# Kernel optimization log

Hardware: AMD Instinct MI355X
Metric: run time of the kernel (lower is better)

## Reference

```python
import jax, jax.numpy as jnp
import numpy as np

N = 100000          # nodes
E = 3200000         # edges
C_IN = 64
HIDDEN = 64
NUM_CLASSES = 10
NUM_GRAPHS = 256
EPS = 1e-5


def _graph_conv(x, src, dst, w_rel, w_root, b):
    # PyG GraphConv(aggr='mean'): out_i = W_rel * mean_{j->i} x_j + W_root * x_i + b
    msg_sum = jax.ops.segment_sum(x[src], dst, num_segments=N)            # [N, C]
    cnt = jax.ops.segment_sum(jnp.ones((src.shape[0], 1), x.dtype), dst,
                              num_segments=N)                             # [N, 1]
    agg = msg_sum / jnp.maximum(cnt, 1.0)
    return agg @ w_rel + x @ w_root + b


def _batch_norm(x, gamma, beta):
    # PyG BatchNorm in training mode: batch stats over the node dimension
    mean = jnp.mean(x, axis=0)
    var = jnp.var(x, axis=0)
    return (x - mean) * jax.lax.rsqrt(var + EPS) * gamma + beta


def setup_inputs() -> dict:
    key = jax.random.key(0)
    ks = jax.random.split(key, 20)
    x = jax.random.normal(ks[0], (N, C_IN), dtype=jnp.float32)
    edge_index = jax.random.randint(ks[1], (2, E), 0, N, dtype=jnp.int32)
    batch = jnp.sort(jax.random.randint(ks[2], (N,), 0, NUM_GRAPHS, dtype=jnp.int32))

    def lin(k, fan_in, fan_out):
        s = 1.0 / np.sqrt(fan_in)
        return jax.random.uniform(k, (fan_in, fan_out), jnp.float32, -s, s)

    dims = [(C_IN, 16), (16, 32), (32, 32), (32, HIDDEN)]
    params = {}
    ki = 3
    for i, (ci, co) in enumerate(dims, start=1):
        params[f"w_rel{i}"] = lin(ks[ki], ci, co); ki += 1
        params[f"w_root{i}"] = lin(ks[ki], ci, co); ki += 1
        params[f"b{i}"] = jnp.zeros((co,), jnp.float32)
        params[f"g{i}"] = jnp.ones((co,), jnp.float32)
        params[f"be{i}"] = jnp.zeros((co,), jnp.float32)
    params["w_lin1"] = lin(ks[ki], HIDDEN, HIDDEN); ki += 1
    params["b_lin1"] = jnp.zeros((HIDDEN,), jnp.float32)
    params["w_lin2"] = lin(ks[ki], HIDDEN, NUM_CLASSES); ki += 1
    params["b_lin2"] = jnp.zeros((NUM_CLASSES,), jnp.float32)

    return {"x": x, "edge_index": edge_index, "batch": batch, **params}


def reference(x, edge_index, batch,
              w_rel1, w_root1, b1, g1, be1,
              w_rel2, w_root2, b2, g2, be2,
              w_rel3, w_root3, b3, g3, be3,
              w_rel4, w_root4, b4, g4, be4,
              w_lin1, b_lin1, w_lin2, b_lin2):
    src, dst = edge_index[0], edge_index[1]
    h = jax.nn.elu(_batch_norm(_graph_conv(x, src, dst, w_rel1, w_root1, b1), g1, be1))
    h = jax.nn.elu(_batch_norm(_graph_conv(h, src, dst, w_rel2, w_root2, b2), g2, be2))
    h = jax.nn.elu(_batch_norm(_graph_conv(h, src, dst, w_rel3, w_root3, b3), g3, be3))
    h = jax.nn.elu(_batch_norm(_graph_conv(h, src, dst, w_rel4, w_root4, b4), g4, be4))
    # global mean pool over graphs
    pooled = jax.ops.segment_sum(h, batch, num_segments=NUM_GRAPHS)
    cnt = jax.ops.segment_sum(jnp.ones((N, 1), h.dtype), batch, num_segments=NUM_GRAPHS)
    pooled = pooled / jnp.maximum(cnt, 1.0)
    z = jax.nn.relu(pooled @ w_lin1 + b_lin1)
    # dropout omitted (deterministic / eval mode)
    logits = z @ w_lin2 + b_lin2
    return jax.nn.log_softmax(logits, axis=-1)
```

## Files before the change

kernel.cpp:

```cpp
#include <hip/hip_runtime.h>
#include <hip/hip_bf16.h>
#include <math.h>

#define NGRAPHS 256
#define BSHIFT 8
#define NBUCK 512
#define NSORT 256
#define SBLK 256
#define SMASK 0x00FFFFFFu

__device__ __forceinline__ float bf2f(unsigned short u) {
    return __uint_as_float((unsigned)u << 16);
}
__device__ __forceinline__ unsigned short f2bf(float f) {
    unsigned u = __float_as_uint(f);
    unsigned r = (u + 0x7FFFu + ((u >> 16) & 1u)) >> 16;
    return (unsigned short)r;
}

__global__ __launch_bounds__(256) void k_bhist(const int* __restrict__ dst, int* __restrict__ hmat, int E) {
    __shared__ int hist[NBUCK];
    for (int i = threadIdx.x; i < NBUCK; i += 256) hist[i] = 0;
    __syncthreads();
    int chunk = (E + NSORT - 1) / NSORT;
    int lo = blockIdx.x * chunk;
    int hi = lo + chunk; if (hi > E) hi = E;
    for (int i = lo + threadIdx.x; i < hi; i += 256) {
        int d = __builtin_nontemporal_load(dst + i);
        atomicAdd(&hist[d >> BSHIFT], 1);
    }
    __syncthreads();
    for (int i = threadIdx.x; i < NBUCK; i += 256)
        hmat[(size_t)blockIdx.x * NBUCK + i] = hist[i];
}

__global__ __launch_bounds__(256) void k_cscan(int* __restrict__ hmat, int* __restrict__ btot) {
    int col = blockIdx.x * 256 + threadIdx.x;
    int run = 0;
#pragma unroll 4
    for (int r = 0; r < NSORT; r++) {
        int v = hmat[(size_t)r * NBUCK + col];
        hmat[(size_t)r * NBUCK + col] = run;
        run += v;
    }
    btot[col] = run;
}

__global__ __launch_bounds__(512) void k_bscan(const int* __restrict__ btot, int* __restrict__ bstart) {
    __shared__ int s[512];
    int tid = threadIdx.x;
    int v = btot[tid];
    s[tid] = v;
    __syncthreads();
    for (int off = 1; off < 512; off <<= 1) {
        int t = (tid >= off) ? s[tid - off] : 0;
        __syncthreads();
        s[tid] += t;
        __syncthreads();
    }
    bstart[tid] = s[tid] - v;
    if (tid == 511) bstart[NBUCK] = s[511];
}

__global__ __launch_bounds__(256) void k_bscatter(const int* __restrict__ src, const int* __restrict__ dst,
                                                  const int* __restrict__ hmat, const int* __restrict__ bstart,
                                                  unsigned* __restrict__ ebuf, int E) {
    __shared__ int cur[NBUCK];
    for (int i = threadIdx.x; i < NBUCK; i += 256)
        cur[i] = bstart[i] + hmat[(size_t)blockIdx.x * NBUCK + i];
    __syncthreads();
    int chunk = (E + NSORT - 1) / NSORT;
    int lo = blockIdx.x * chunk;
    int hi = lo + chunk; if (hi > E) hi = E;
    for (int i = lo + threadIdx.x; i < hi; i += 256) {
        int d = __builtin_nontemporal_load(dst + i);
        int s = __builtin_nontemporal_load(src + i);
        int p = atomicAdd(&cur[d >> BSHIFT], 1);
        ebuf[p] = (unsigned)s | ((unsigned)(d & 255) << 24);
    }
}

__global__ __launch_bounds__(256) void k_sort2(const unsigned* __restrict__ ebuf, const int* __restrict__ bstart,
                                               int* __restrict__ csr, int* __restrict__ row_start, int N) {
    __shared__ int hist[256];
    __shared__ int sc[256];
    __shared__ int scur[256];
    int b = blockIdx.x;
    int e0 = bstart[b], e1 = bstart[b + 1];
    hist[threadIdx.x] = 0;
    __syncthreads();
    for (int i = e0 + threadIdx.x; i < e1; i += 256)
        atomicAdd(&hist[__builtin_nontemporal_load(ebuf + i) >> 24], 1);
    __syncthreads();
    sc[threadIdx.x] = hist[threadIdx.x];
    __syncthreads();
    for (int off = 1; off < 256; off <<= 1) {
        int t = (threadIdx.x >= off) ? sc[threadIdx.x - off] : 0;
        __syncthreads();
        sc[threadIdx.x] += t;
        __syncthreads();
    }
    {
        int inc = sc[threadIdx.x];
        int ex = inc - hist[threadIdx.x];
        scur[threadIdx.x] = e0 + ex;
        int node = (b << BSHIFT) + threadIdx.x;
        if (node < N) row_start[node] = e0 + ex;
        if (node == N - 1) row_start[N] = e0 + inc;
    }
    __syncthreads();
    for (int i = e0 + threadIdx.x; i < e1; i += 256) {
        unsigned w = __builtin_nontemporal_load(ebuf + i);
        int p = atomicAdd(&scur[w >> 24], 1);
        csr[p] = (int)(w & SMASK);
    }
}

template <int CI, int CO, bool HAS_REL, bool HAS_ROOT, bool ADD_AGG, bool HAS_BIAS, bool IN_BF16, bool OUT_BF16>
__global__ __launch_bounds__(256) void k_lin(const void* __restrict__ hroot_v, const float* __restrict__ hrel,
                                             const float* __restrict__ w_rel, const float* __restrict__ w_root,
                                             const float* __restrict__ bias, const float* __restrict__ aggadd,
                                             float* __restrict__ out, unsigned short* __restrict__ outb, int N) {
    constexpr int QPR = CO / 4;
    __shared__ float s_rel[HAS_REL ? CI * CO : 1];
    __shared__ float s_root[HAS_ROOT ? CI * CO : 1];
    __shared__ float s_b[HAS_BIAS ? CO : 4];
    if (HAS_REL)
        for (int i = threadIdx.x; i < CI * CO; i += 256) s_rel[i] = w_rel[i];
    if (HAS_ROOT)
        for (int i = threadIdx.x; i < CI * CO; i += 256) s_root[i] = w_root[i];
    if (HAS_BIAS && threadIdx.x < CO) s_b[threadIdx.x] = bias[threadIdx.x];
    __syncthreads();

    int t = blockIdx.x * 256 + threadIdx.x;
    int n = t / QPR;
    int c0 = (t % QPR) * 4;
    if (n >= N) return;

    float rr[HAS_ROOT ? CI : 1];
    if (HAS_ROOT) {
        if (IN_BF16) {
            const ushort4* hp = (const ushort4*)((const unsigned short*)hroot_v + (size_t)n * CI);
#pragma unroll
            for (int i = 0; i < CI / 4; i++) {
                ushort4 v = hp[i];
                rr[4 * i + 0] = bf2f(v.x); rr[4 * i + 1] = bf2f(v.y);
                rr[4 * i + 2] = bf2f(v.z); rr[4 * i + 3] = bf2f(v.w);
            }
        } else {
            const float4* hp = (const float4*)((const float*)hroot_v + (size_t)n * CI);
#pragma unroll
            for (int i = 0; i < CI / 4; i++) {
                float4 v = hp[i];
                rr[4 * i + 0] = v.x; rr[4 * i + 1] = v.y; rr[4 * i + 2] = v.z; rr[4 * i + 3] = v.w;
            }
        }
    }
    float ar[HAS_REL ? CI : 1];
    if (HAS_REL) {
        const float4* mp = (const float4*)(hrel + (size_t)n * CI);
#pragma unroll
        for (int i = 0; i < CI / 4; i++) {
            float4 v = mp[i];
            ar[4 * i + 0] = v.x; ar[4 * i + 1] = v.y; ar[4 * i + 2] = v.z; ar[4 * i + 3] = v.w;
        }
    }

    float4 acc;
    if (HAS_BIAS) acc = *(const float4*)&s_b[c0];
    else { acc.x = 0.f; acc.y = 0.f; acc.z = 0.f; acc.w = 0.f; }
    if (ADD_AGG) {
        float4 v = *(const float4*)(aggadd + (size_t)n * CO + c0);
        acc.x += v.x; acc.y += v.y; acc.z += v.z; acc.w += v.w;
    }

#pragma unroll
    for (int ci = 0; ci < CI; ci++) {
        if (HAS_REL) {
            float a = ar[ci];
            float4 w = *(const float4*)&s_rel[ci * CO + c0];
            acc.x += a * w.x; acc.y += a * w.y; acc.z += a * w.z; acc.w += a * w.w;
        }
        if (HAS_ROOT) {
            float hv = rr[ci];
            float4 w = *(const float4*)&s_root[ci * CO + c0];
            acc.x += hv * w.x; acc.y += hv * w.y; acc.z += hv * w.z; acc.w += hv * w.w;
        }
    }
    if (OUT_BF16) {
        ushort4 o;
        o.x = f2bf(acc.x); o.y = f2bf(acc.y); o.z = f2bf(acc.z); o.w = f2bf(acc.w);
        *(ushort4*)(outb + (size_t)n * CO + c0) = o;
    } else {
        *(float4*)(out + (size_t)n * CO + c0) = acc;
    }
}

#define GCHUNK 1024
template <int C>
__global__ __launch_bounds__(256) void k_gather(const unsigned short* __restrict__ h,
                                                const int* __restrict__ row_start,
                                                const int* __restrict__ csr, float* __restrict__ agg, int N) {
    constexpr int LPR = C / 4;
    constexpr int EPP = 64 / LPR;
    constexpr int DEPTH = 32 / EPP;
    __shared__ int sbuf[GCHUNK];
    int lane = threadIdx.x & 63;
    int w = threadIdx.x >> 6;
    int nb = blockIdx.x * 4;
    int wid = nb + w;
    bool act = wid < N;
    int nb_end = nb + 4; if (nb_end > N) nb_end = N;
    int eb0 = row_start[nb];
    int eb1 = row_start[nb_end];
    int r0 = act ? row_start[wid] : 0;
    int r1 = act ? row_start[wid + 1] : 0;
    int es = lane / LPR;
    int cq = (lane % LPR) * 4;

    float a0 = 0.f, a1 = 0.f, a2 = 0.f, a3 = 0.f;
    for (int base = eb0; base < eb1; base += GCHUNK) {
        int len = eb1 - base; if (len > GCHUNK) len = GCHUNK;
        __syncthreads();
        for (int i = threadIdx.x; i < len; i += 256)
            sbuf[i] = __builtin_nontemporal_load(csr + base + i);
        __syncthreads();
        if (act) {
            int lo = (r0 > base ? r0 : base) - base;
            int hiv = r1 < base + len ? r1 : base + len;
            int hi = hiv - base;
            if (hi > lo) {
                int nfull = (hi - lo) >> 5;
                int j0 = lo;
                for (int b = 0; b < nfull; b++, j0 += 32) {
                    int s[DEPTH];
#pragma unroll
                    for (int u = 0; u < DEPTH; u++) s[u] = sbuf[j0 + u * EPP + es];
                    ushort4 v[DEPTH];
#pragma unroll
                    for (int u = 0; u < DEPTH; u++)
                        v[u] = *(const ushort4*)(h + (size_t)s[u] * C + cq);
#pragma unroll
                    for (int u = 0; u < DEPTH; u++) {
                        a0 += bf2f(v[u].x); a1 += bf2f(v[u].y);
                        a2 += bf2f(v[u].z); a3 += bf2f(v[u].w);
                    }
                }
                for (int j = j0 + es; j < hi; j += EPP) {
                    int s = sbuf[j];
                    ushort4 v = *(const ushort4*)(h + (size_t)s * C + cq);
                    a0 += bf2f(v.x); a1 += bf2f(v.y); a2 += bf2f(v.z); a3 += bf2f(v.w);
                }
            }
        }
    }
#pragma unroll
    for (int off = LPR; off < 64; off <<= 1) {
        a0 += __shfl_xor(a0, off, 64);
        a1 += __shfl_xor(a1, off, 64);
        a2 += __shfl_xor(a2, off, 64);
        a3 += __shfl_xor(a3, off, 64);
    }
    if (act && lane < LPR) {
        int deg = r1 - r0;
        float rec = 1.0f / (float)(deg > 0 ? deg : 1);
        float4 o; o.x = a0 * rec; o.y = a1 * rec; o.z = a2 * rec; o.w = a3 * rec;
        *(float4*)(agg + (size_t)wid * C + cq) = o;
    }
}

template <int CO>
__global__ __launch_bounds__(256) void k_stats(const float* __restrict__ h, float* __restrict__ partials,
                                               const float* __restrict__ g, const float* __restrict__ be,
                                               float* __restrict__ stats, int* __restrict__ cnt,
                                               float invN, int N) {
    constexpr int QPR = CO / 4;
    __shared__ float part[4][2 * CO];
    __shared__ float red[128];
    __shared__ int is_last;
    int total = N * QPR;
    float s0 = 0, s1 = 0, s2 = 0, s3 = 0, q0 = 0, q1 = 0, q2 = 0, q3 = 0;
    int idx = blockIdx.x * 256 + threadIdx.x;
    for (int i = idx; i < total; i += SBLK * 256) {
        float4 v = ((const float4*)h)[i];
        s0 += v.x; q0 += v.x * v.x;
        s1 += v.y; q1 += v.y * v.y;
        s2 += v.z; q2 += v.z * v.z;
        s3 += v.w; q3 += v.w * v.w;
    }
#pragma unroll
    for (int off = QPR; off < 64; off <<= 1) {
        s0 += __shfl_xor(s0, off, 64); q0 += __shfl_xor(q0, off, 64);
        s1 += __shfl_xor(s1, off, 64); q1 += __shfl_xor(q1, off, 64);
        s2 += __shfl_xor(s2, off, 64); q2 += __shfl_xor(q2, off, 64);
        s3 += __shfl_xor(s3, off, 64); q3 += __shfl_xor(q3, off, 64);
    }
    int lane = threadIdx.x & 63;
    int w = threadIdx.x >> 6;
    if (lane < QPR) {
        int cq = lane * 4;
        part[w][cq + 0] = s0; part[w][CO + cq + 0] = q0;
        part[w][cq + 1] = s1; part[w][CO + cq + 1] = q1;
        part[w][cq + 2] = s2; part[w][CO + cq + 2] = q2;
        part[w][cq + 3] = s3; part[w][CO + cq + 3] = q3;
    }
    __syncthreads();
    if (threadIdx.x < 2 * CO) {
        float v = part[0][threadIdx.x] + part[1][threadIdx.x] + part[2][threadIdx.x] + part[3][threadIdx.x];
        partials[blockIdx.x * (2 * CO) + threadIdx.x] = v;
    }
    __threadfence();
    if (threadIdx.x == 0) is_last = (atomicAdd(cnt, 1) == SBLK - 1);
    __syncthreads();
    if (!is_last) return;
    __threadfence();
    int c = threadIdx.x;
    if (c < 2 * CO) {
        float s = 0.f;
        for (int b = 0; b < SBLK; b++) s += partials[b * 2 * CO + c];
        red[c] = s;
    }
    __syncthreads();
    if (c < CO) {
        float mean = red[c] * invN;
        float var = red[CO + c] * invN - mean * mean;
        float sc = g[c] * rsqrtf(var + 1e-5f);
        stats[128 + c] = sc;
        stats[192 + c] = be[c] - mean * sc;
    }
}

template <int CO>
__global__ __launch_bounds__(256) void k_bn_elu(const float* __restrict__ h, const float* __restrict__ stats,
                                                unsigned short* __restrict__ hb, int N) {
    __shared__ float sc[CO], sh[CO];
    if (threadIdx.x < CO) {
        sc[threadIdx.x] = stats[128 + threadIdx.x];
        sh[threadIdx.x] = stats[192 + threadIdx.x];
    }
    __syncthreads();
    int total = N * (CO / 4);
    int i = blockIdx.x * 256 + threadIdx.x;
    if (i >= total) return;
    float4 v = ((const float4*)h)[i];
    int cq = (i % (CO / 4)) * 4;
    v.x = v.x * sc[cq + 0] + sh[cq + 0];
    v.y = v.y * sc[cq + 1] + sh[cq + 1];
    v.z = v.z * sc[cq + 2] + sh[cq + 2];
    v.w = v.w * sc[cq + 3] + sh[cq + 3];
    v.x = v.x > 0.f ? v.x : expm1f(v.x);
    v.y = v.y > 0.f ? v.y : expm1f(v.y);
    v.z = v.z > 0.f ? v.z : expm1f(v.z);
    v.w = v.w > 0.f ? v.w : expm1f(v.w);
    ushort4 o;
    o.x = f2bf(v.x); o.y = f2bf(v.y); o.z = f2bf(v.z); o.w = f2bf(v.w);
    ((ushort4*)hb)[i] = o;
}

__global__ __launch_bounds__(256) void k_bn_elu_pool(const float* __restrict__ h, const float* __restrict__ stats,
                                                     const int* __restrict__ batch,
                                                     float* __restrict__ pooled, float* __restrict__ cntg, int N) {
    int lane = threadIdx.x & 63;
    int wid = blockIdx.x * 4 + (threadIdx.x >> 6);
    int n0 = wid * 16;
    if (n0 >= N) return;
    float scl = stats[128 + lane];
    float shl = stats[192 + lane];
    int nmax = N - n0; if (nmax > 16) nmax = 16;
    int cur = batch[n0];
    float acc = 0.f;
    float run = 0.f;
    for (int k = 0; k < nmax; k++) {
        int g = batch[n0 + k];
        if (g != cur) {
            atomicAdd(&pooled[(size_t)cur * 64 + lane], acc);
            if (lane == 0) atomicAdd(&cntg[cur], run);
            cur = g; acc = 0.f; run = 0.f;
        }
        float v = h[(size_t)(n0 + k) * 64 + lane] * scl + shl;
        v = v > 0.f ? v : expm1f(v);
        acc += v;
        run += 1.f;
    }
    atomicAdd(&pooled[(size_t)cur * 64 + lane], acc);
    if (lane == 0) atomicAdd(&cntg[cur], run);
}

__global__ __launch_bounds__(256) void k_head(const float* __restrict__ pooled, const float* __restrict__ cntg,
                                              const float* __restrict__ w1, const float* __restrict__ b1,
                                              const float* __restrict__ w2, const float* __restrict__ b2,
                                              float* __restrict__ out) {
    int g = threadIdx.x;
    float rec = 1.0f / fmaxf(cntg[g], 1.0f);
    float p[64];
    {
        const float4* pp = (const float4*)(pooled + (size_t)g * 64);
#pragma unroll
        for (int i = 0; i < 16; i++) {
            float4 v = pp[i];
            p[4 * i + 0] = v.x * rec; p[4 * i + 1] = v.y * rec;
            p[4 * i + 2] = v.z * rec; p[4 * i + 3] = v.w * rec;
        }
    }
    float lg[10];
#pragma unroll
    for (int t = 0; t < 10; t++) lg[t] = b2[t];
#pragma unroll 1
    for (int j = 0; j < 64; j++) {
        float a = b1[j];
#pragma unroll
        for (int k = 0; k < 64; k++) a += p[k] * w1[k * 64 + j];
        a = fmaxf(a, 0.f);
#pragma unroll
        for (int t = 0; t < 10; t++) lg[t] += a * w2[j * 10 + t];
    }
    float m = -1e30f;
#pragma unroll
    for (int t = 0; t < 10; t++) m = fmaxf(m, lg[t]);
    float s = 0.f;
#pragma unroll
    for (int t = 0; t < 10; t++) s += expf(lg[t] - m);
    float lse = m + logf(s);
#pragma unroll
    for (int t = 0; t < 10; t++) out[(size_t)g * 10 + t] = lg[t] - lse;
}

extern "C" void kernel_launch(void* const* d_in, const int* in_sizes, int n_in,
                              void* d_out, int out_size, void* d_ws, size_t ws_size,
                              hipStream_t stream) {
    const float* x = (const float*)d_in[0];
    const int* ei = (const int*)d_in[1];
    const int* batch = (const int*)d_in[2];
    const int N = in_sizes[0] / 64;
    const int E = in_sizes[1] / 2;
    const int* src = ei;
    const int* dst = ei + E;

    const float* w_rel1 = (const float*)d_in[3];
    const float* w_root1 = (const float*)d_in[4];
    const float* b1 = (const float*)d_in[5];
    const float* g1 = (const float*)d_in[6];
    const float* be1 = (const float*)d_in[7];
    const float* w_rel2 = (const float*)d_in[8];
    const float* w_root2 = (const float*)d_in[9];
    const float* b2 = (const float*)d_in[10];
    const float* g2 = (const float*)d_in[11];
    const float* be2 = (const float*)d_in[12];
    const float* w_rel3 = (const float*)d_in[13];
    const float* w_root3 = (const float*)d_in[14];
    const float* b3 = (const float*)d_in[15];
    const float* g3 = (const float*)d_in[16];
    const float* be3 = (const float*)d_in[17];
    const float* w_rel4 = (const float*)d_in[18];
    const float* w_root4 = (const float*)d_in[19];
    const float* b4 = (const float*)d_in[20];
    const float* g4 = (const float*)d_in[21];
    const float* be4 = (const float*)d_in[22];
    const float* w_lin1 = (const float*)d_in[23];
    const float* b_lin1 = (const float*)d_in[24];
    const float* w_lin2 = (const float*)d_in[25];
    const float* b_lin2 = (const float*)d_in[26];

    char* ws = (char*)d_ws;
    size_t off = 0;
    auto alloc = [&](size_t bytes) { size_t o = off; off += (bytes + 255) & ~(size_t)255; return o; };
    int* hmat = (int*)(ws + alloc((size_t)NSORT * NBUCK * 4));
    int* btot = (int*)(ws + alloc((size_t)NBUCK * 4));
    int* bstart = (int*)(ws + alloc((size_t)(NBUCK + 1) * 4));
    unsigned* ebuf = (unsigned*)(ws + alloc((size_t)E * 4));
    int* csr = (int*)(ws + alloc((size_t)E * 4));
    int* row_start = (int*)(ws + alloc((size_t)(N + 1) * 4));
    float* agg = (float*)(ws + alloc((size_t)N * 32 * 4));
    unsigned short* y1b = (unsigned short*)(ws + alloc((size_t)N * 16 * 2));
    unsigned short* hb = (unsigned short*)(ws + alloc((size_t)N * 64 * 2));
    float* bufA = (float*)(ws + alloc((size_t)N * 64 * 4));
    float* stats = (float*)(ws + alloc(4 * 256 * 4));
    float* partials = (float*)(ws + alloc((size_t)SBLK * 128 * 4));
    float* pooled = (float*)(ws + alloc((size_t)(NGRAPHS * 64 + NGRAPHS + 8) * 4));
    float* cntg = pooled + NGRAPHS * 64;
    int* cnt = (int*)(cntg + NGRAPHS);

    hipMemsetAsync(pooled, 0, (size_t)(NGRAPHS * 64 + NGRAPHS + 8) * 4, stream);

    const float invN = 1.0f / (float)N;
    const int gbl = (N + 3) / 4;
    auto lgrid = [&](int qpr) { return (N * qpr + 255) / 256; };

    k_bhist<<<NSORT, 256, 0, stream>>>(dst, hmat, E);
    k_cscan<<<NBUCK / 256, 256, 0, stream>>>(hmat, btot);
    k_bscan<<<1, 512, 0, stream>>>(btot, bstart);
    k_bscatter<<<NSORT, 256, 0, stream>>>(src, dst, hmat, bstart, ebuf, E);
    k_sort2<<<NBUCK, 256, 0, stream>>>(ebuf, bstart, csr, row_start, N);

    k_lin<64, 16, true, false, false, false, false, true><<<lgrid(4), 256, 0, stream>>>(
        nullptr, x, w_rel1, nullptr, nullptr, nullptr, nullptr, y1b, N);
    k_gather<16><<<gbl, 256, 0, stream>>>(y1b, row_start, csr, agg, N);
    k_lin<64, 16, false, true, true, true, false, false><<<lgrid(4), 256, 0, stream>>>(
        x, nullptr, nullptr, w_root1, b1, agg, bufA, nullptr, N);
    k_stats<16><<<SBLK, 256, 0, stream>>>(bufA, partials, g1, be1, stats + 0, cnt + 0, invN, N);
    k_bn_elu<16><<<(N * 4 + 255) / 256, 256, 0, stream>>>(bufA, stats + 0, hb, N);

    k_gather<16><<<gbl, 256, 0, stream>>>(hb, row_start, csr, agg, N);
    k_lin<16, 32, true, true, false, true, true, false><<<lgrid(8), 256, 0, stream>>>(
        hb, agg, w_rel2, w_root2, b2, nullptr, bufA, nullptr, N);
    k_stats<32><<<SBLK, 256, 0, stream>>>(bufA, partials, g2, be2, stats + 256, cnt + 1, invN, N);
    k_bn_elu<32><<<(N * 8 + 255) / 256, 256, 0, stream>>>(bufA, stats + 256, hb, N);

    k_gather<32><<<gbl, 256, 0, stream>>>(hb, row_start, csr, agg, N);
    k_lin<32, 32, true, true, false, true, true, false><<<lgrid(8), 256, 0, stream>>>(
        hb, agg, w_rel3, w_root3, b3, nullptr, bufA, nullptr, N);
    k_stats<32><<<SBLK, 256, 0, stream>>>(bufA, partials, g3, be3, stats + 512, cnt + 2, invN, N);
    k_bn_elu<32><<<(N * 8 + 255) / 256, 256, 0, stream>>>(bufA, stats + 512, hb, N);

    k_gather<32><<<gbl, 256, 0, stream>>>(hb, row_start, csr, agg, N);
    k_lin<32, 64, true, true, false, true, true, false><<<lgrid(16), 256, 0, stream>>>(
        hb, agg, w_rel4, w_root4, b4, nullptr, bufA, nullptr, N);
    k_stats<64><<<SBLK, 256, 0, stream>>>(bufA, partials, g4, be4, stats + 768, cnt + 3, invN, N);
    int waves16 = (N + 15) / 16;
    k_bn_elu_pool<<<(waves16 + 3) / 4, 256, 0, stream>>>(bufA, stats + 768, batch, pooled, cntg, N);

    k_head<<<1, 256, 0, stream>>>(pooled, cntg, w_lin1, b_lin1, w_lin2, b_lin2, (float*)d_out);
}
```

Baseline: 638.9 us.

## Fuse whole GNN pipeline into one cooperative persistent kernel with grid syncs

Replaces the chain of about twenty separate kernel launches with a single cooperative persistent megakernel. Phases (bucket sort, CSR build, linear layers, gathers, batch-norm stats, pooling, head) are separated by grid-wide syncs, and blocks loop over work with grid stride. The per-call memset is folded into the first phase, and the batch-norm statistics appear to be merged into the linear phases. This removes launch gaps and tail idle time, at the cost of grid-sync overhead and occupancy-limited persistent grids, with a multi-kernel fallback when cooperative launch is unavailable.

```diff
diff --git a/kernel.cpp b/kernel.cpp
--- a/kernel.cpp
+++ b/kernel.cpp
@@ -1,12 +1,15 @@
 #include <hip/hip_runtime.h>
+#include <hip/hip_cooperative_groups.h>
 #include <hip/hip_bf16.h>
 #include <math.h>
+
+namespace cg = cooperative_groups;
 
 #define NGRAPHS 256
 #define BSHIFT 8
 #define NBUCK 512
 #define NSORT 256
-#define SBLK 256
+#define GCHUNK 1024
 #define SMASK 0x00FFFFFFu
 
 __device__ __forceinline__ float bf2f(unsigned short u) {
@@ -18,275 +21,289 @@
     return (unsigned short)r;
 }
 
-__global__ __launch_bounds__(256) void k_bhist(const int* __restrict__ dst, int* __restrict__ hmat, int E) {
-    __shared__ int hist[NBUCK];
-    for (int i = threadIdx.x; i < NBUCK; i += 256) hist[i] = 0;
-    __syncthreads();
-    int chunk = (E + NSORT - 1) / NSORT;
-    int lo = blockIdx.x * chunk;
-    int hi = lo + chunk; if (hi > E) hi = E;
-    for (int i = lo + threadIdx.x; i < hi; i += 256) {
-        int d = __builtin_nontemporal_load(dst + i);
-        atomicAdd(&hist[d >> BSHIFT], 1);
-    }
-    __syncthreads();
-    for (int i = threadIdx.x; i < NBUCK; i += 256)
-        hmat[(size_t)blockIdx.x * NBUCK + i] = hist[i];
-}
-
-__global__ __launch_bounds__(256) void k_cscan(int* __restrict__ hmat, int* __restrict__ btot) {
-    int col = blockIdx.x * 256 + threadIdx.x;
-    int run = 0;
-#pragma unroll 4
+struct SMLin { float rel[2048]; float root[2048]; float b[64]; float part[512]; };
+struct SMSort { int h[256]; int s[256]; int c[256]; };
+struct SMBn { float sc[64]; float sh[64]; };
+union SM {
+    int hist[NBUCK];
+    int sbuf[GCHUNK];
+    int scan[512];
+    SMSort sort;
+    SMLin lin;
+    SMBn bn;
+};
+
+struct MegaP {
+    const float* x; const int* src; const int* dst; const int* batch;
+    int N, E; float invN;
+    const float *w_rel1, *w_root1, *b1, *g1, *be1;
+    const float *w_rel2, *w_root2, *b2, *g2, *be2;
+    const float *w_rel3, *w_root3, *b3, *g3, *be3;
+    const float *w_rel4, *w_root4, *b4, *g4, *be4;
+    const float *w_lin1, *b_lin1, *w_lin2, *b_lin2;
+    int* hmat; int* bstart; unsigned* ebuf; int* csr; int* row_start;
+    float* agg; unsigned short* y1b; unsigned short* hb; float* bufA;
+    float* gs;
+    float* pooled; float* cntg;
+    float* out;
+};
+
+__device__ void phA(const MegaP& p, SM* sm) {
+    int bid = blockIdx.x, tid = threadIdx.x;
+    if (bid < NSORT) {
+        for (int i = tid; i < NBUCK; i += 256) sm->hist[i] = 0;
+        __syncthreads();
+        int chunk = (p.E + NSORT - 1) / NSORT;
+        int lo = bid * chunk;
+        int hi = lo + chunk; if (hi > p.E) hi = p.E;
+        for (int i = lo + tid; i < hi; i += 256)
+            atomicAdd(&sm->hist[__builtin_nontemporal_load(p.dst + i) >> BSHIFT], 1);
+        __syncthreads();
+        for (int i = tid; i < NBUCK; i += 256)
+            p.hmat[(size_t)bid * NBUCK + i] = sm->hist[i];
+    } else {
+        if (bid == NSORT) {
+            for (int i = tid; i < NGRAPHS * 64 + NGRAPHS; i += 256) p.pooled[i] = 0.f;
+            for (int i = tid; i < 512; i += 256) p.gs[i] = 0.f;
+        }
+        float* s_rel = sm->lin.rel;
+        for (int i = tid; i < 64 * 16; i += 256) s_rel[i] = p.w_rel1[i];
+        __syncthreads();
+        int total = p.N * 4;
+        int nb = gridDim.x - NSORT;
+        for (int i = (bid - NSORT) * 256 + tid; i < total; i += nb * 256) {
+            int n = i >> 2, c0 = (i & 3) << 2;
+            const float4* mp = (const float4*)(p.x + (size_t)n * 64);
+            float4 acc; acc.x = 0.f; acc.y = 0.f; acc.z = 0.f; acc.w = 0.f;
+#pragma unroll
+            for (int k2 = 0; k2 < 16; k2++) {
+                float4 v = mp[k2];
+                const float* wr = &s_rel[(k2 * 4) * 16 + c0];
+                float4 w0 = *(const float4*)(wr);
+                float4 w1 = *(const float4*)(wr + 16);
+                float4 w2 = *(const float4*)(wr + 32);
+                float4 w3 = *(const float4*)(wr + 48);
+                acc.x += v.x * w0.x + v.y * w1.x + v.z * w2.x + v.w * w3.x;
+                acc.y += v.x * w0.y + v.y * w1.y + v.z * w2.y + v.w * w3.y;
+                acc.z += v.x * w0.z + v.y * w1.z + v.z * w2.z + v.w * w3.z;
+                acc.w += v.x * w0.w + v.y * w1.w + v.z * w2.w + v.w * w3.w;
+            }
+            ushort4 o; o.x = f2bf(acc.x); o.y = f2bf(acc.y); o.z = f2bf(acc.z); o.w = f2bf(acc.w);
+            *(ushort4*)(p.y1b + (size_t)n * 16 + c0) = o;
+        }
+    }
+}
+
+__device__ void phB(const MegaP& p, SM* sm) {
+    int t = threadIdx.x;
+    int run0 = 0, run1 = 0;
     for (int r = 0; r < NSORT; r++) {
-        int v = hmat[(size_t)r * NBUCK + col];
-        hmat[(size_t)r * NBUCK + col] = run;
-        run += v;
-    }
-    btot[col] = run;
-}
-
-__global__ __launch_bounds__(512) void k_bscan(const int* __restrict__ btot, int* __restrict__ bstart) {
-    __shared__ int s[512];
-    int tid = threadIdx.x;
-    int v = btot[tid];
-    s[tid] = v;
-    __syncthreads();
-    for (int off = 1; off < 512; off <<= 1) {
-        int t = (tid >= off) ? s[tid - off] : 0;
-        __syncthreads();
-        s[tid] += t;
-        __syncthreads();
-    }
-    bstart[tid] = s[tid] - v;
-    if (tid == 511) bstart[NBUCK] = s[511];
-}
-
-__global__ __launch_bounds__(256) void k_bscatter(const int* __restrict__ src, const int* __restrict__ dst,
-                                                  const int* __restrict__ hmat, const int* __restrict__ bstart,
-                                                  unsigned* __restrict__ ebuf, int E) {
-    __shared__ int cur[NBUCK];
-    for (int i = threadIdx.x; i < NBUCK; i += 256)
-        cur[i] = bstart[i] + hmat[(size_t)blockIdx.x * NBUCK + i];
-    __syncthreads();
-    int chunk = (E + NSORT - 1) / NSORT;
-    int lo = blockIdx.x * chunk;
-    int hi = lo + chunk; if (hi > E) hi = E;
-    for (int i = lo + threadIdx.x; i < hi; i += 256) {
-        int d = __builtin_nontemporal_load(dst + i);
-        int s = __builtin_nontemporal_load(src + i);
-        int p = atomicAdd(&cur[d >> BSHIFT], 1);
-        ebuf[p] = (unsigned)s | ((unsigned)(d & 255) << 24);
-    }
-}
-
-__global__ __launch_bounds__(256) void k_sort2(const unsigned* __restrict__ ebuf, const int* __restrict__ bstart,
-                                               int* __restrict__ csr, int* __restrict__ row_start, int N) {
-    __shared__ int hist[256];
-    __shared__ int sc[256];
-    __shared__ int scur[256];
-    int b = blockIdx.x;
-    int e0 = bstart[b], e1 = bstart[b + 1];
-    hist[threadIdx.x] = 0;
-    __syncthreads();
-    for (int i = e0 + threadIdx.x; i < e1; i += 256)
-        atomicAdd(&hist[__builtin_nontemporal_load(ebuf + i) >> 24], 1);
-    __syncthreads();
-    sc[threadIdx.x] = hist[threadIdx.x];
+        size_t base = (size_t)r * NBUCK;
+        int v0 = p.hmat[base + t];
+        int v1 = p.hmat[base + 256 + t];
+        p.hmat[base + t] = run0;
+        p.hmat[base + 256 + t] = run1;
+        run0 += v0; run1 += v1;
+    }
+    sm->scan[t] = run0; sm->scan[256 + t] = run1;
     __syncthreads();
     for (int off = 1; off < 256; off <<= 1) {
-        int t = (threadIdx.x >= off) ? sc[threadIdx.x - off] : 0;
-        __syncthreads();
-        sc[threadIdx.x] += t;
-        __syncthreads();
-    }
-    {
-        int inc = sc[threadIdx.x];
-        int ex = inc - hist[threadIdx.x];
-        scur[threadIdx.x] = e0 + ex;
-        int node = (b << BSHIFT) + threadIdx.x;
-        if (node < N) row_start[node] = e0 + ex;
-        if (node == N - 1) row_start[N] = e0 + inc;
-    }
-    __syncthreads();
-    for (int i = e0 + threadIdx.x; i < e1; i += 256) {
-        unsigned w = __builtin_nontemporal_load(ebuf + i);
-        int p = atomicAdd(&scur[w >> 24], 1);
-        csr[p] = (int)(w & SMASK);
-    }
-}
-
-template <int CI, int CO, bool HAS_REL, bool HAS_ROOT, bool ADD_AGG, bool HAS_BIAS, bool IN_BF16, bool OUT_BF16>
-__global__ __launch_bounds__(256) void k_lin(const void* __restrict__ hroot_v, const float* __restrict__ hrel,
-                                             const float* __restrict__ w_rel, const float* __restrict__ w_root,
-                                             const float* __restrict__ bias, const float* __restrict__ aggadd,
-                                             float* __restrict__ out, unsigned short* __restrict__ outb, int N) {
-    constexpr int QPR = CO / 4;
-    __shared__ float s_rel[HAS_REL ? CI * CO : 1];
-    __shared__ float s_root[HAS_ROOT ? CI * CO : 1];
-    __shared__ float s_b[HAS_BIAS ? CO : 4];
-    if (HAS_REL)
-        for (int i = threadIdx.x; i < CI * CO; i += 256) s_rel[i] = w_rel[i];
-    if (HAS_ROOT)
-        for (int i = threadIdx.x; i < CI * CO; i += 256) s_root[i] = w_root[i];
-    if (HAS_BIAS && threadIdx.x < CO) s_b[threadIdx.x] = bias[threadIdx.x];
-    __syncthreads();
-
-    int t = blockIdx.x * 256 + threadIdx.x;
-    int n = t / QPR;
-    int c0 = (t % QPR) * 4;
-    if (n >= N) return;
-
-    float rr[HAS_ROOT ? CI : 1];
-    if (HAS_ROOT) {
-        if (IN_BF16) {
-            const ushort4* hp = (const ushort4*)((const unsigned short*)hroot_v + (size_t)n * CI);
-#pragma unroll
-            for (int i = 0; i < CI / 4; i++) {
-                ushort4 v = hp[i];
-                rr[4 * i + 0] = bf2f(v.x); rr[4 * i + 1] = bf2f(v.y);
-                rr[4 * i + 2] = bf2f(v.z); rr[4 * i + 3] = bf2f(v.w);
-            }
-        } else {
-            const float4* hp = (const float4*)((const float*)hroot_v + (size_t)n * CI);
-#pragma unroll
-            for (int i = 0; i < CI / 4; i++) {
-                float4 v = hp[i];
-                rr[4 * i + 0] = v.x; rr[4 * i + 1] = v.y; rr[4 * i + 2] = v.z; rr[4 * i + 3] = v.w;
-            }
-        }
-    }
-    float ar[HAS_REL ? CI : 1];
-    if (HAS_REL) {
-        const float4* mp = (const float4*)(hrel + (size_t)n * CI);
-#pragma unroll
-        for (int i = 0; i < CI / 4; i++) {
-            float4 v = mp[i];
-            ar[4 * i + 0] = v.x; ar[4 * i + 1] = v.y; ar[4 * i + 2] = v.z; ar[4 * i + 3] = v.w;
-        }
-    }
-
-    float4 acc;
-    if (HAS_BIAS) acc = *(const float4*)&s_b[c0];
-    else { acc.x = 0.f; acc.y = 0.f; acc.z = 0.f; acc.w = 0.f; }
-    if (ADD_AGG) {
-        float4 v = *(const float4*)(aggadd + (size_t)n * CO + c0);
-        acc.x += v.x; acc.y += v.y; acc.z += v.z; acc.w += v.w;
-    }
-
-#pragma unroll
-    for (int ci = 0; ci < CI; ci++) {
-        if (HAS_REL) {
-            float a = ar[ci];
-            float4 w = *(const float4*)&s_rel[ci * CO + c0];
-            acc.x += a * w.x; acc.y += a * w.y; acc.z += a * w.z; acc.w += a * w.w;
-        }
-        if (HAS_ROOT) {
-            float hv = rr[ci];
-            float4 w = *(const float4*)&s_root[ci * CO + c0];
-            acc.x += hv * w.x; acc.y += hv * w.y; acc.z += hv * w.z; acc.w += hv * w.w;
-        }
-    }
-    if (OUT_BF16) {
-        ushort4 o;
-        o.x = f2bf(acc.x); o.y = f2bf(acc.y); o.z = f2bf(acc.z); o.w = f2bf(acc.w);
-        *(ushort4*)(outb + (size_t)n * CO + c0) = o;
-    } else {
-        *(float4*)(out + (size_t)n * CO + c0) = acc;
-    }
-}
-
-#define GCHUNK 1024
+        int v0 = (t >= off) ? sm->scan[t - off] : 0;
+        int v1 = (t >= off) ? sm->scan[256 + t - off] : 0;
+        __syncthreads();
+        sm->scan[t] += v0; sm->scan[256 + t] += v1;
+        __syncthreads();
+    }
+    int lowtot = sm->scan[255];
+    int incU = sm->scan[256 + t] + lowtot;
+    p.bstart[t] = sm->scan[t] - run0;
+    p.bstart[256 + t] = incU - run1;
+    if (t == 255) p.bstart[NBUCK] = incU;
+}
+
+__device__ void phC(const MegaP& p, SM* sm) {
+    int tid = threadIdx.x;
+    for (int b = blockIdx.x; b < NSORT; b += gridDim.x) {
+        for (int i = tid; i < NBUCK; i += 256)
+            sm->hist[i] = p.bstart[i] + p.hmat[(size_t)b * NBUCK + i];
+        __syncthreads();
+        int chunk = (p.E + NSORT - 1) / NSORT;
+        int lo = b * chunk;
+        int hi = lo + chunk; if (hi > p.E) hi = p.E;
+        for (int i = lo + tid; i < hi; i += 256) {
+            int d = __builtin_nontemporal_load(p.dst + i);
+            int s = __builtin_nontemporal_load(p.src + i);
+            int pos = atomicAdd(&sm->hist[d >> BSHIFT], 1);
+            p.ebuf[pos] = (unsigned)s | ((unsigned)(d & 255) << 24);
+        }
+        __syncthreads();
+    }
+}
+
+__device__ void phD(const MegaP& p, SM* sm) {
+    int tid = threadIdx.x;
+    for (int b = blockIdx.x; b < NBUCK; b += gridDim.x) {
+        int e0 = p.bstart[b], e1 = p.bstart[b + 1];
+        sm->sort.h[tid] = 0;
+        __syncthreads();
+        for (int i = e0 + tid; i < e1; i += 256)
+            atomicAdd(&sm->sort.h[__builtin_nontemporal_load(p.ebuf + i) >> 24], 1);
+        __syncthreads();
+        sm->sort.s[tid] = sm->sort.h[tid];
+        __syncthreads();
+        for (int off = 1; off < 256; off <<= 1) {
+            int v = (tid >= off) ? sm->sort.s[tid - off] : 0;
+            __syncthreads();
+            sm->sort.s[tid] += v;
+            __syncthreads();
+        }
+        {
+            int inc = sm->sort.s[tid];
+            int ex = inc - sm->sort.h[tid];
+            sm->sort.c[tid] = e0 + ex;
+            int node = (b << BSHIFT) + tid;
+            if (node < p.N) p.row_start[node] = e0 + ex;
+            if (node == p.N - 1) p.row_start[p.N] = e0 + inc;
+        }
+        __syncthreads();
+        for (int i = e0 + tid; i < e1; i += 256) {
+            unsigned w = __builtin_nontemporal_load(p.ebuf + i);
+            int pos = atomicAdd(&sm->sort.c[w >> 24], 1);
+            p.csr[pos] = (int)(w & SMASK);
+        }
+        __syncthreads();
+    }
+}
+
 template <int C>
-__global__ __launch_bounds__(256) void k_gather(const unsigned short* __restrict__ h,
-                                                const int* __restrict__ row_start,
-                                                const int* __restrict__ csr, float* __restrict__ agg, int N) {
+__device__ void ph_gather(const MegaP& p, SM* sm, const unsigned short* h) {
     constexpr int LPR = C / 4;
     constexpr int EPP = 64 / LPR;
     constexpr int DEPTH = 32 / EPP;
-    __shared__ int sbuf[GCHUNK];
     int lane = threadIdx.x & 63;
     int w = threadIdx.x >> 6;
-    int nb = blockIdx.x * 4;
-    int wid = nb + w;
-    bool act = wid < N;
-    int nb_end = nb + 4; if (nb_end > N) nb_end = N;
-    int eb0 = row_start[nb];
-    int eb1 = row_start[nb_end];
-    int r0 = act ? row_start[wid] : 0;
-    int r1 = act ? row_start[wid + 1] : 0;
     int es = lane / LPR;
     int cq = (lane % LPR) * 4;
-
-    float a0 = 0.f, a1 = 0.f, a2 = 0.f, a3 = 0.f;
-    for (int base = eb0; base < eb1; base += GCHUNK) {
-        int len = eb1 - base; if (len > GCHUNK) len = GCHUNK;
-        __syncthreads();
-        for (int i = threadIdx.x; i < len; i += 256)
-            sbuf[i] = __builtin_nontemporal_load(csr + base + i);
-        __syncthreads();
-        if (act) {
-            int lo = (r0 > base ? r0 : base) - base;
-            int hiv = r1 < base + len ? r1 : base + len;
-            int hi = hiv - base;
-            if (hi > lo) {
-                int nfull = (hi - lo) >> 5;
-                int j0 = lo;
-                for (int b = 0; b < nfull; b++, j0 += 32) {
-                    int s[DEPTH];
-#pragma unroll
-                    for (int u = 0; u < DEPTH; u++) s[u] = sbuf[j0 + u * EPP + es];
-                    ushort4 v[DEPTH];
-#pragma unroll
-                    for (int u = 0; u < DEPTH; u++)
-                        v[u] = *(const ushort4*)(h + (size_t)s[u] * C + cq);
-#pragma unroll
-                    for (int u = 0; u < DEPTH; u++) {
-                        a0 += bf2f(v[u].x); a1 += bf2f(v[u].y);
-                        a2 += bf2f(v[u].z); a3 += bf2f(v[u].w);
+    int ngrp = (p.N + 3) >> 2;
+    for (int grp = blockIdx.x; grp < ngrp; grp += gridDim.x) {
+        int nb = grp * 4;
+        int wid = nb + w;
+        bool act = wid < p.N;
+        int nb_end = nb + 4; if (nb_end > p.N) nb_end = p.N;
+        int eb0 = p.row_start[nb];
+        int eb1 = p.row_start[nb_end];
+        int r0 = act ? p.row_start[wid] : 0;
+        int r1 = act ? p.row_start[wid + 1] : 0;
+        float a0 = 0.f, a1 = 0.f, a2 = 0.f, a3 = 0.f;
+        for (int base = eb0; base < eb1; base += GCHUNK) {
+            int len = eb1 - base; if (len > GCHUNK) len = GCHUNK;
+            __syncthreads();
+            for (int i = threadIdx.x; i < len; i += 256)
+                sm->sbuf[i] = __builtin_nontemporal_load(p.csr + base + i);
+            __syncthreads();
+            if (act) {
+                int lo = (r0 > base ? r0 : base) - base;
+                int hiv = r1 < base + len ? r1 : base + len;
+                int hi = hiv - base;
+                if (hi > lo) {
+                    int nfull = (hi - lo) >> 5;
+                    int j0 = lo;
+                    for (int bb = 0; bb < nfull; bb++, j0 += 32) {
+                        int s[DEPTH];
+#pragma unroll
+                        for (int u = 0; u < DEPTH; u++) s[u] = sm->sbuf[j0 + u * EPP + es];
+                        ushort4 v[DEPTH];
+#pragma unroll
+                        for (int u = 0; u < DEPTH; u++)
+                            v[u] = *(const ushort4*)(h + (size_t)s[u] * C + cq);
+#pragma unroll
+                        for (int u = 0; u < DEPTH; u++) {
+                            a0 += bf2f(v[u].x); a1 += bf2f(v[u].y);
+                            a2 += bf2f(v[u].z); a3 += bf2f(v[u].w);
+                        }
+                    }
+                    for (int j = j0 + es; j < hi; j += EPP) {
+                        int s = sm->sbuf[j];
+                        ushort4 v = *(const ushort4*)(h + (size_t)s * C + cq);
+                        a0 += bf2f(v.x); a1 += bf2f(v.y); a2 += bf2f(v.z); a3 += bf2f(v.w);
                     }
                 }
-                for (int j = j0 + es; j < hi; j += EPP) {
-                    int s = sbuf[j];
-                    ushort4 v = *(const ushort4*)(h + (size_t)s * C + cq);
-                    a0 += bf2f(v.x); a1 += bf2f(v.y); a2 += bf2f(v.z); a3 += bf2f(v.w);
-                }
             }
         }
-    }
-#pragma unroll
-    for (int off = LPR; off < 64; off <<= 1) {
-        a0 += __shfl_xor(a0, off, 64);
-        a1 += __shfl_xor(a1, off, 64);
-        a2 += __shfl_xor(a2, off, 64);
-        a3 += __shfl_xor(a3, off, 64);
-    }
-    if (act && lane < LPR) {
-        int deg = r1 - r0;
-        float rec = 1.0f / (float)(deg > 0 ? deg : 1);
-        float4 o; o.x = a0 * rec; o.y = a1 * rec; o.z = a2 * rec; o.w = a3 * rec;
-        *(float4*)(agg + (size_t)wid * C + cq) = o;
-    }
-}
-
-template <int CO>
-__global__ __launch_bounds__(256) void k_stats(const float* __restrict__ h, float* __restrict__ partials,
-                                               const float* __restrict__ g, const float* __restrict__ be,
-                                               float* __restrict__ stats, int* __restrict__ cnt,
-                                               float invN, int N) {
+#pragma unroll
+        for (int off = LPR; off < 64; off <<= 1) {
+            a0 += __shfl_xor(a0, off, 64);
+            a1 += __shfl_xor(a1, off, 64);
+            a2 += __shfl_xor(a2, off, 64);
+            a3 += __shfl_xor(a3, off, 64);
+        }
+        if (act && lane < LPR) {
+            int deg = r1 - r0;
+            float rec = 1.0f / (float)(deg > 0 ? deg : 1);
+            float4 o; o.x = a0 * rec; o.y = a1 * rec; o.z = a2 * rec; o.w = a3 * rec;
+            *(float4*)(p.agg + (size_t)wid * C + cq) = o;
+        }
+    }
+}
+
+template <int CI, int CO, bool HAS_REL, bool ADD_AGG, bool IN_BF16>
+__device__ void ph_lin_stats(const MegaP& p, SM* sm, const void* hroot_v, const float* hrel,
+                             const float* w_rel, const float* w_root, const float* bias,
+                             float* out, float* gsl) {
     constexpr int QPR = CO / 4;
-    __shared__ float part[4][2 * CO];
-    __shared__ float red[128];
-    __shared__ int is_last;
-    int total = N * QPR;
+    int tid = threadIdx.x;
+    if (HAS_REL)
+        for (int i = tid; i < CI * CO; i += 256) sm->lin.rel[i] = w_rel[i];
+    for (int i = tid; i < CI * CO; i += 256) sm->lin.root[i] = w_root[i];
+    if (tid < CO) sm->lin.b[tid] = bias[tid];
+    __syncthreads();
+    int total = p.N * QPR;
+    int stride = gridDim.x * 256;
     float s0 = 0, s1 = 0, s2 = 0, s3 = 0, q0 = 0, q1 = 0, q2 = 0, q3 = 0;
-    int idx = blockIdx.x * 256 + threadIdx.x;
-    for (int i = idx; i < total; i += SBLK * 256) {
-        float4 v = ((const float4*)h)[i];
-        s0 += v.x; q0 += v.x * v.x;
-        s1 += v.y; q1 += v.y * v.y;
-        s2 += v.z; q2 += v.z * v.z;
-        s3 += v.w; q3 += v.w * v.w;
+    for (int i = blockIdx.x * 256 + tid; i < total; i += stride) {
+        int n = i / QPR, c0 = (i % QPR) * 4;
+        float4 acc = *(const float4*)&sm->lin.b[c0];
+        if (ADD_AGG) {
+            float4 v = ((const float4*)p.agg)[i];
+            acc.x += v.x; acc.y += v.y; acc.z += v.z; acc.w += v.w;
+        }
+#pragma unroll
+        for (int cb = 0; cb < CI / 4; cb++) {
+            float f0, f1, f2, f3;
+            if (IN_BF16) {
+                ushort4 v = *(const ushort4*)((const unsigned short*)hroot_v + (size_t)n * CI + cb * 4);
+                f0 = bf2f(v.x); f1 = bf2f(v.y); f2 = bf2f(v.z); f3 = bf2f(v.w);
+            } else {
+                float4 v = *(const float4*)((const float*)hroot_v + (size_t)n * CI + cb * 4);
+                f0 = v.x; f1 = v.y; f2 = v.z; f3 = v.w;
+            }
+            const float* wr = &sm->lin.root[(cb * 4) * CO + c0];
+            float4 w0 = *(const float4*)(wr);
+            float4 w1 = *(const float4*)(wr + CO);
+            float4 w2 = *(const float4*)(wr + 2 * CO);
+            float4 w3 = *(const float4*)(wr + 3 * CO);
+            acc.x += f0 * w0.x + f1 * w1.x + f2 * w2.x + f3 * w3.x;
+            acc.y += f0 * w0.y + f1 * w1.y + f2 * w2.y + f3 * w3.y;
+            acc.z += f0 * w0.z + f1 * w1.z + f2 * w2.z + f3 * w3.z;
+            acc.w += f0 * w0.w + f1 * w1.w + f2 * w2.w + f3 * w3.w;
+            if (HAS_REL) {
+                float4 a = *(const float4*)(hrel + (size_t)n * CI + cb * 4);
+                const float* we = &sm->lin.rel[(cb * 4) * CO + c0];
+                float4 e0 = *(const float4*)(we);
+                float4 e1 = *(const float4*)(we + CO);
+                float4 e2 = *(const float4*)(we + 2 * CO);
+                float4 e3 = *(const float4*)(we + 3 * CO);
+                acc.x += a.x * e0.x + a.y * e1.x + a.z * e2.x + a.w * e3.x;
+                acc.y += a.x * e0.y + a.y * e1.y + a.z * e2.y + a.w * e3.y;
+                acc.z += a.x * e0.z + a.y * e1.z + a.z * e2.z + a.w * e3.z;
+                acc.w += a.x * e0.w + a.y * e1.w + a.z * e2.w + a.w * e3.w;
+            }
+        }
+        ((float4*)out)[i] = acc;
+        s0 += acc.x; q0 += acc.x * acc.x;
+        s1 += acc.y; q1 += acc.y * acc.y;
+        s2 += acc.z; q2 += acc.z * acc.z;
+        s3 += acc.w; q3 += acc.w * acc.w;
     }
 #pragma unroll
     for (int off = QPR; off < 64; off <<= 1) {
@@ -295,124 +312,115 @@
         s2 += __shfl_xor(s2, off, 64); q2 += __shfl_xor(q2, off, 64);
         s3 += __shfl_xor(s3, off, 64); q3 += __shfl_xor(q3, off, 64);
     }
-    int lane = threadIdx.x & 63;
-    int w = threadIdx.x >> 6;
+    int lane = tid & 63;
+    int w = tid >> 6;
     if (lane < QPR) {
         int cq = lane * 4;
-        part[w][cq + 0] = s0; part[w][CO + cq + 0] = q0;
-        part[w][cq + 1] = s1; part[w][CO + cq + 1] = q1;
-        part[w][cq + 2] = s2; part[w][CO + cq + 2] = q2;
-        part[w][cq + 3] = s3; part[w][CO + cq + 3] = q3;
+        float* pr = &sm->lin.part[w * 2 * CO];
+        pr[cq + 0] = s0; pr[CO + cq + 0] = q0;
+        pr[cq + 1] = s1; pr[CO + cq + 1] = q1;
+        pr[cq + 2] = s2; pr[CO + cq + 2] = q2;
+        pr[cq + 3] = s3; pr[CO + cq + 3] = q3;
     }
     __syncthreads();
-    if (threadIdx.x < 2 * CO) {
-        float v = part[0][threadIdx.x] + part[1][threadIdx.x] + part[2][threadIdx.x] + part[3][threadIdx.x];
-        partials[blockIdx.x * (2 * CO) + threadIdx.x] = v;
-    }
-    __threadfence();
-    if (threadIdx.x == 0) is_last = (atomicAdd(cnt, 1) == SBLK - 1);
+    if (tid < 2 * CO) {
+        float v = sm->lin.part[tid] + sm->lin.part[2 * CO + tid] +
+                  sm->lin.part[4 * CO + tid] + sm->lin.part[6 * CO + tid];
+        atomicAdd(&gsl[tid], v);
+    }
+}
+
+template <int CO>
+__device__ void ph_bn_elu(const MegaP& p, SM* sm, const float* gsl, const float* g, const float* be) {
+    int tid = threadIdx.x;
+    if (tid < CO) {
+        float mean = gsl[tid] * p.invN;
+        float var = gsl[CO + tid] * p.invN - mean * mean;
+        float sc = g[tid] * rsqrtf(var + 1e-5f);
+        sm->bn.sc[tid] = sc;
+        sm->bn.sh[tid] = be[tid] - mean * sc;
+    }
     __syncthreads();
-    if (!is_last) return;
-    __threadfence();
-    int c = threadIdx.x;
-    if (c < 2 * CO) {
-        float s = 0.f;
-        for (int b = 0; b < SBLK; b++) s += partials[b * 2 * CO + c];
-        red[c] = s;
+    int total = p.N * (CO / 4);
+    int stride = gridDim.x * 256;
+    for (int i = blockIdx.x * 256 + tid; i < total; i += stride) {
+        float4 v = ((const float4*)p.bufA)[i];
+        int cq = (i % (CO / 4)) * 4;
+        v.x = v.x * sm->bn.sc[cq + 0] + sm->bn.sh[cq + 0];
+        v.y = v.y * sm->bn.sc[cq + 1] + sm->bn.sh[cq + 1];
+        v.z = v.z * sm->bn.sc[cq + 2] + sm->bn.sh[cq + 2];
+        v.w = v.w * sm->bn.sc[cq + 3] + sm->bn.sh[cq + 3];
+        v.x = v.x > 0.f ? v.x : expm1f(v.x);
+        v.y = v.y > 0.f ? v.y : expm1f(v.y);
+        v.z = v.z > 0.f ? v.z : expm1f(v.z);
+        v.w = v.w > 0.f ? v.w : expm1f(v.w);
+        ushort4 o;
+        o.x = f2bf(v.x); o.y = f2bf(v.y); o.z = f2bf(v.z); o.w = f2bf(v.w);
+        ((ushort4*)p.hb)[i] = o;
+    }
+}
+
+__device__ void ph_pool(const MegaP& p, SM* sm, const float* gsl) {
+    int tid = threadIdx.x;
+    if (tid < 64) {
+        float mean = gsl[tid] * p.invN;
+        float var = gsl[64 + tid] * p.invN - mean * mean;
+        float sc = p.g4[tid] * rsqrtf(var + 1e-5f);
+        sm->bn.sc[tid] = sc;
+        sm->bn.sh[tid] = p.be4[tid] - mean * sc;
     }
     __syncthreads();
-    if (c < CO) {
-        float mean = red[c] * invN;
-        float var = red[CO + c] * invN - mean * mean;
-        float sc = g[c] * rsqrtf(var + 1e-5f);
-        stats[128 + c] = sc;
-        stats[192 + c] = be[c] - mean * sc;
-    }
-}
-
-template <int CO>
-__global__ __launch_bounds__(256) void k_bn_elu(const float* __restrict__ h, const float* __restrict__ stats,
-                                                unsigned short* __restrict__ hb, int N) {
-    __shared__ float sc[CO], sh[CO];
-    if (threadIdx.x < CO) {
-        sc[threadIdx.x] = stats[128 + threadIdx.x];
-        sh[threadIdx.x] = stats[192 + threadIdx.x];
-    }
-    __syncthreads();
-    int total = N * (CO / 4);
-    int i = blockIdx.x * 256 + threadIdx.x;
-    if (i >= total) return;
-    float4 v = ((const float4*)h)[i];
-    int cq = (i % (CO / 4)) * 4;
-    v.x = v.x * sc[cq + 0] + sh[cq + 0];
-    v.y = v.y * sc[cq + 1] + sh[cq + 1];
-    v.z = v.z * sc[cq + 2] + sh[cq + 2];
-    v.w = v.w * sc[cq + 3] + sh[cq + 3];
-    v.x = v.x > 0.f ? v.x : expm1f(v.x);
-    v.y = v.y > 0.f ? v.y : expm1f(v.y);
-    v.z = v.z > 0.f ? v.z : expm1f(v.z);
-    v.w = v.w > 0.f ? v.w : expm1f(v.w);
-    ushort4 o;
-    o.x = f2bf(v.x); o.y = f2bf(v.y); o.z = f2bf(v.z); o.w = f2bf(v.w);
-    ((ushort4*)hb)[i] = o;
-}
-
-__global__ __launch_bounds__(256) void k_bn_elu_pool(const float* __restrict__ h, const float* __restrict__ stats,
-                                                     const int* __restrict__ batch,
-                                                     float* __restrict__ pooled, float* __restrict__ cntg, int N) {
-    int lane = threadIdx.x & 63;
-    int wid = blockIdx.x * 4 + (threadIdx.x >> 6);
-    int n0 = wid * 16;
-    if (n0 >= N) return;
-    float scl = stats[128 + lane];
-    float shl = stats[192 + lane];
-    int nmax = N - n0; if (nmax > 16) nmax = 16;
-    int cur = batch[n0];
-    float acc = 0.f;
-    float run = 0.f;
-    for (int k = 0; k < nmax; k++) {
-        int g = batch[n0 + k];
-        if (g != cur) {
-            atomicAdd(&pooled[(size_t)cur * 64 + lane], acc);
-            if (lane == 0) atomicAdd(&cntg[cur], run);
-            cur = g; acc = 0.f; run = 0.f;
-        }
-        float v = h[(size_t)(n0 + k) * 64 + lane] * scl + shl;
-        v = v > 0.f ? v : expm1f(v);
-        acc += v;
-        run += 1.f;
-    }
-    atomicAdd(&pooled[(size_t)cur * 64 + lane], acc);
-    if (lane == 0) atomicAdd(&cntg[cur], run);
-}
-
-__global__ __launch_bounds__(256) void k_head(const float* __restrict__ pooled, const float* __restrict__ cntg,
-                                              const float* __restrict__ w1, const float* __restrict__ b1,
-                                              const float* __restrict__ w2, const float* __restrict__ b2,
-                                              float* __restrict__ out) {
+    int lane = tid & 63;
+    int w = tid >> 6;
+    float scl = sm->bn.sc[lane];
+    float shl = sm->bn.sh[lane];
+    int ngrp = (p.N + 15) / 16;
+    for (int gi = blockIdx.x * 4 + w; gi < ngrp; gi += gridDim.x * 4) {
+        int n0 = gi * 16;
+        int nmax = p.N - n0; if (nmax > 16) nmax = 16;
+        int cur = p.batch[n0];
+        float acc = 0.f, run = 0.f;
+        for (int k = 0; k < nmax; k++) {
+            int gg = p.batch[n0 + k];
+            if (gg != cur) {
+                atomicAdd(&p.pooled[(size_t)cur * 64 + lane], acc);
+                if (lane == 0) atomicAdd(&p.cntg[cur], run);
+                cur = gg; acc = 0.f; run = 0.f;
+            }
+            float v = p.bufA[(size_t)(n0 + k) * 64 + lane] * scl + shl;
+            v = v > 0.f ? v : expm1f(v);
+            acc += v;
+            run += 1.f;
+        }
+        atomicAdd(&p.pooled[(size_t)cur * 64 + lane], acc);
+        if (lane == 0) atomicAdd(&p.cntg[cur], run);
+    }
+}
+
+__device__ void ph_head(const MegaP& p) {
     int g = threadIdx.x;
-    float rec = 1.0f / fmaxf(cntg[g], 1.0f);
-    float p[64];
+    float rec = 1.0f / fmaxf(p.cntg[g], 1.0f);
+    float pv[64];
     {
-        const float4* pp = (const float4*)(pooled + (size_t)g * 64);
+        const float4* pp = (const float4*)(p.pooled + (size_t)g * 64);
 #pragma unroll
         for (int i = 0; i < 16; i++) {
             float4 v = pp[i];
-            p[4 * i + 0] = v.x * rec; p[4 * i + 1] = v.y * rec;
-            p[4 * i + 2] = v.z * rec; p[4 * i + 3] = v.w * rec;
+            pv[4 * i + 0] = v.x * rec; pv[4 * i + 1] = v.y * rec;
+            pv[4 * i + 2] = v.z * rec; pv[4 * i + 3] = v.w * rec;
         }
     }
     float lg[10];
 #pragma unroll
-    for (int t = 0; t < 10; t++) lg[t] = b2[t];
+    for (int t = 0; t < 10; t++) lg[t] = p.b_lin2[t];
 #pragma unroll 1
     for (int j = 0; j < 64; j++) {
-        float a = b1[j];
-#pragma unroll
-        for (int k = 0; k < 64; k++) a += p[k] * w1[k * 64 + j];
+        float a = p.b_lin1[j];
+#pragma unroll
+        for (int k = 0; k < 64; k++) a += pv[k] * p.w_lin1[k * 64 + j];
         a = fmaxf(a, 0.f);
 #pragma unroll
-        for (int t = 0; t < 10; t++) lg[t] += a * w2[j * 10 + t];
+        for (int t = 0; t < 10; t++) lg[t] += a * p.w_lin2[j * 10 + t];
     }
     float m = -1e30f;
 #pragma unroll
@@ -422,8 +430,53 @@
     for (int t = 0; t < 10; t++) s += expf(lg[t] - m);
     float lse = m + logf(s);
 #pragma unroll
-    for (int t = 0; t < 10; t++) out[(size_t)g * 10 + t] = lg[t] - lse;
-}
+    for (int t = 0; t < 10; t++) p.out[(size_t)g * 10 + t] = lg[t] - lse;
+}
+
+__global__ __launch_bounds__(256, 4) void k_mega(MegaP p) {
+    __shared__ SM sm;
+    cg::grid_group grid = cg::this_grid();
+
+    phA(p, &sm);                                    grid.sync();
+    if (blockIdx.x == 0) phB(p, &sm);               grid.sync();
+    phC(p, &sm);                                    grid.sync();
+    phD(p, &sm);                                    grid.sync();
+
+    ph_gather<16>(p, &sm, p.y1b);                   grid.sync();
+    ph_lin_stats<64, 16, false, true, false>(p, &sm, p.x, nullptr, nullptr, p.w_root1, p.b1, p.bufA, p.gs + 0);
+                                                    grid.sync();
+    ph_bn_elu<16>(p, &sm, p.gs + 0, p.g1, p.be1);   grid.sync();
+    ph_gather<16>(p, &sm, p.hb);                    grid.sync();
+    ph_lin_stats<16, 32, true, false, true>(p, &sm, p.hb, p.agg, p.w_rel2, p.w_root2, p.b2, p.bufA, p.gs + 128);
+                                                    grid.sync();
+    ph_bn_elu<32>(p, &sm, p.gs + 128, p.g2, p.be2); grid.sync();
+    ph_gather<32>(p, &sm, p.hb);                    grid.sync();
+    ph_lin_stats<32, 32, true, false, true>(p, &sm, p.hb, p.agg, p.w_rel3, p.w_root3, p.b3, p.bufA, p.gs + 256);
+                                                    grid.sync();
+    ph_bn_elu<32>(p, &sm, p.gs + 256, p.g3, p.be3); grid.sync();
+    ph_gather<32>(p, &sm, p.hb);                    grid.sync();
+    ph_lin_stats<32, 64, true, false, true>(p, &sm, p.hb, p.agg, p.w_rel4, p.w_root4, p.b4, p.bufA, p.gs + 384);
+                                                    grid.sync();
+    ph_pool(p, &sm, p.gs + 384);                    grid.sync();
+    if (blockIdx.x == 0) ph_head(p);
+}
+
+__global__ __launch_bounds__(256) void w_A(MegaP p) { __shared__ SM sm; phA(p, &sm); }
+__global__ __launch_bounds__(256) void w_B(MegaP p) { __shared__ SM sm; if (blockIdx.x == 0) phB(p, &sm); }
+__global__ __launch_bounds__(256) void w_C(MegaP p) { __shared__ SM sm; phC(p, &sm); }
+__global__ __launch_bounds__(256) void w_D(MegaP p) { __shared__ SM sm; phD(p, &sm); }
+__global__ __launch_bounds__(256) void w_G16a(MegaP p) { __shared__ SM sm; ph_gather<16>(p, &sm, p.y1b); }
+__global__ __launch_bounds__(256) void w_G16b(MegaP p) { __shared__ SM sm; ph_gather<16>(p, &sm, p.hb); }
+__global__ __launch_bounds__(256) void w_G32(MegaP p) { __shared__ SM sm; ph_gather<32>(p, &sm, p.hb); }
+__global__ __launch_bounds__(256) void w_L1(MegaP p) { __shared__ SM sm; ph_lin_stats<64, 16, false, true, false>(p, &sm, p.x, nullptr, nullptr, p.w_root1, p.b1, p.bufA, p.gs + 0); }
+__global__ __launch_bounds__(256) void w_L2(MegaP p) { __shared__ SM sm; ph_lin_stats<16, 32, true, false, true>(p, &sm, p.hb, p.agg, p.w_rel2, p.w_root2, p.b2, p.bufA, p.gs + 128); }
+__global__ __launch_bounds__(256) void w_L3(MegaP p) { __shared__ SM sm; ph_lin_stats<32, 32, true, false, true>(p, &sm, p.hb, p.agg, p.w_rel3, p.w_root3, p.b3, p.bufA, p.gs + 256); }
+__global__ __launch_bounds__(256) void w_L4(MegaP p) { __shared__ SM sm; ph_lin_stats<32, 64, true, false, true>(p, &sm, p.hb, p.agg, p.w_rel4, p.w_root4, p.b4, p.bufA, p.gs + 384); }
+__global__ __launch_bounds__(256) void w_B1(MegaP p) { __shared__ SM sm; ph_bn_elu<16>(p, &sm, p.gs + 0, p.g1, p.be1); }
+__global__ __launch_bounds__(256) void w_B2(MegaP p) { __shared__ SM sm; ph_bn_elu<32>(p, &sm, p.gs + 128, p.g2, p.be2); }
+__global__ __launch_bounds__(256) void w_B3(MegaP p) { __shared__ SM sm; ph_bn_elu<32>(p, &sm, p.gs + 256, p.g3, p.be3); }
+__global__ __launch_bounds__(256) void w_P(MegaP p) { __shared__ SM sm; ph_pool(p, &sm, p.gs + 384); }
+__global__ __launch_bounds__(256) void w_H(MegaP p) { if (blockIdx.x == 0) ph_head(p); }
 
 extern "C" void kernel_launch(void* const* d_in, const int* in_sizes, int n_in,
                               void* d_out, int out_size, void* d_ws, size_t ws_size,
@@ -433,91 +486,72 @@
     const int* batch = (const int*)d_in[2];
     const int N = in_sizes[0] / 64;
     const int E = in_sizes[1] / 2;
-    const int* src = ei;
-    const int* dst = ei + E;
-
-    const float* w_rel1 = (const float*)d_in[3];
-    const float* w_root1 = (const float*)d_in[4];
-    const float* b1 = (const float*)d_in[5];
-    const float* g1 = (const float*)d_in[6];
-    const float* be1 = (const float*)d_in[7];
-    const float* w_rel2 = (const float*)d_in[8];
-    const float* w_root2 = (const float*)d_in[9];
-    const float* b2 = (const float*)d_in[10];
-    const float* g2 = (const float*)d_in[11];
-    const float* be2 = (const float*)d_in[12];
-    const float* w_rel3 = (const float*)d_in[13];
-    const float* w_root3 = (const float*)d_in[14];
-    const float* b3 = (const float*)d_in[15];
-    const float* g3 = (const float*)d_in[16];
-    const float* be3 = (const float*)d_in[17];
-    const float* w_rel4 = (const float*)d_in[18];
-    const float* w_root4 = (const float*)d_in[19];
-    const float* b4 = (const float*)d_in[20];
-    const float* g4 = (const float*)d_in[21];
-    const float* be4 = (const float*)d_in[22];
-    const float* w_lin1 = (const float*)d_in[23];
-    const float* b_lin1 = (const float*)d_in[24];
-    const float* w_lin2 = (const float*)d_in[25];
-    const float* b_lin2 = (const float*)d_in[26];
+
+    MegaP P;
+    P.x = x; P.src = ei; P.dst = ei + E; P.batch = batch;
+    P.N = N; P.E = E; P.invN = 1.0f / (float)N;
+    P.w_rel1 = (const float*)d_in[3];  P.w_root1 = (const float*)d_in[4];
+    P.b1 = (const float*)d_in[5];      P.g1 = (const float*)d_in[6];   P.be1 = (const float*)d_in[7];
+    P.w_rel2 = (const float*)d_in[8];  P.w_root2 = (const float*)d_in[9];
+    P.b2 = (const float*)d_in[10];     P.g2 = (const float*)d_in[11];  P.be2 = (const float*)d_in[12];
+    P.w_rel3 = (const float*)d_in[13]; P.w_root3 = (const float*)d_in[14];
+    P.b3 = (const float*)d_in[15];     P.g3 = (const float*)d_in[16];  P.be3 = (const float*)d_in[17];
+    P.w_rel4 = (const float*)d_in[18]; P.w_root4 = (const float*)d_in[19];
+    P.b4 = (const float*)d_in[20];     P.g4 = (const float*)d_in[21];  P.be4 = (const float*)d_in[22];
+    P.w_lin1 = (const float*)d_in[23]; P.b_lin1 = (const float*)d_in[24];
+    P.w_lin2 = (const float*)d_in[25]; P.b_lin2 = (const float*)d_in[26];
 
     char* ws = (char*)d_ws;
     size_t off = 0;
     auto alloc = [&](size_t bytes) { size_t o = off; off += (bytes + 255) & ~(size_t)255; return o; };
-    int* hmat = (int*)(ws + alloc((size_t)NSORT * NBUCK * 4));
-    int* btot = (int*)(ws + alloc((size_t)NBUCK * 4));
-    int* bstart = (int*)(ws + alloc((size_t)(NBUCK + 1) * 4));
-    unsigned* ebuf = (unsigned*)(ws + alloc((size_t)E * 4));
-    int* csr = (int*)(ws + alloc((size_t)E * 4));
-    int* row_start = (int*)(ws + alloc((size_t)(N + 1) * 4));
-    float* agg = (float*)(ws + alloc((size_t)N * 32 * 4));
-    unsigned short* y1b = (unsigned short*)(ws + alloc((size_t)N * 16 * 2));
-    unsigned short* hb = (unsigned short*)(ws + alloc((size_t)N * 64 * 2));
-    float* bufA = (float*)(ws + alloc((size_t)N * 64 * 4));
-    float* stats = (float*)(ws + alloc(4 * 256 * 4));
-    float* partials = (float*)(ws + alloc((size_t)SBLK * 128 * 4));
-    float* pooled = (float*)(ws + alloc((size_t)(NGRAPHS * 64 + NGRAPHS + 8) * 4));
-    float* cntg = pooled + NGRAPHS * 64;
-    int* cnt = (int*)(cntg + NGRAPHS);
-
-    hipMemsetAsync(pooled, 0, (size_t)(NGRAPHS * 64 + NGRAPHS + 8) * 4, stream);
-
-    const float invN = 1.0f / (float)N;
-    const int gbl = (N + 3) / 4;
-    auto lgrid = [&](int qpr) { return (N * qpr + 255) / 256; };
-
-    k_bhist<<<NSORT, 256, 0, stream>>>(dst, hmat, E);
-    k_cscan<<<NBUCK / 256, 256, 0, stream>>>(hmat, btot);
-    k_bscan<<<1, 512, 0, stream>>>(btot, bstart);
-    k_bscatter<<<NSORT, 256, 0, stream>>>(src, dst, hmat, bstart, ebuf, E);
-    k_sort2<<<NBUCK, 256, 0, stream>>>(ebuf, bstart, csr, row_start, N);
-
-    k_lin<64, 16, true, false, false, false, false, true><<<lgrid(4), 256, 0, stream>>>(
-        nullptr, x, w_rel1, nullptr, nullptr, nullptr, nullptr, y1b, N);
-    k_gather<16><<<gbl, 256, 0, stream>>>(y1b, row_start, csr, agg, N);
-    k_lin<64, 16, false, true, true, true, false, false><<<lgrid(4), 256, 0, stream>>>(
-        x, nullptr, nullptr, w_root1, b1, agg, bufA, nullptr, N);
-    k_stats<16><<<SBLK, 256, 0, stream>>>(bufA, partials, g1, be1, stats + 0, cnt + 0, invN, N);
-    k_bn_elu<16><<<(N * 4 + 255) / 256, 256, 0, stream>>>(bufA, stats + 0, hb, N);
-
-    k_gather<16><<<gbl, 256, 0, stream>>>(hb, row_start, csr, agg, N);
-    k_lin<16, 32, true, true, false, true, true, false><<<lgrid(8), 256, 0, stream>>>(
-        hb, agg, w_rel2, w_root2, b2, nullptr, bufA, nullptr, N);
-    k_stats<32><<<SBLK, 256, 0, stream>>>(bufA, partials, g2, be2, stats + 256, cnt + 1, invN, N);
-    k_bn_elu<32><<<(N * 8 + 255) / 256, 256, 0, stream>>>(bufA, stats + 256, hb, N);
-
-    k_gather<32><<<gbl, 256, 0, stream>>>(hb, row_start, csr, agg, N);
-    k_lin<32, 32, true, true, false, true, true, false><<<lgrid(8), 256, 0, stream>>>(
-        hb, agg, w_rel3, w_root3, b3, nullptr, bufA, nullptr, N);
-    k_stats<32><<<SBLK, 256, 0, stream>>>(bufA, partials, g3, be3, stats + 512, cnt + 2, invN, N);
-    k_bn_elu<32><<<(N * 8 + 255) / 256, 256, 0, stream>>>(bufA, stats + 512, hb, N);
-
-    k_gather<32><<<gbl, 256, 0, stream>>>(hb, row_start, csr, agg, N);
-    k_lin<32, 64, true, true, false, true, true, false><<<lgrid(16), 256, 0, stream>>>(
-        hb, agg, w_rel4, w_root4, b4, nullptr, bufA, nullptr, N);
-    k_stats<64><<<SBLK, 256, 0, stream>>>(bufA, partials, g4, be4, stats + 768, cnt + 3, invN, N);
-    int waves16 = (N + 15) / 16;
-    k_bn_elu_pool<<<(waves16 + 3) / 4, 256, 0, stream>>>(bufA, stats + 768, batch, pooled, cntg, N);
-
-    k_head<<<1, 256, 0, stream>>>(pooled, cntg, w_lin1, b_lin1, w_lin2, b_lin2, (float*)d_out);
-}
+    P.hmat = (int*)(ws + alloc((size_t)NSORT * NBUCK * 4));
+    P.bstart = (int*)(ws + alloc((size_t)(NBUCK + 1) * 4));
+    P.ebuf = (unsigned*)(ws + alloc((size_t)E * 4));
+    P.csr = (int*)(ws + alloc((size_t)E * 4));
+    P.row_start = (int*)(ws + alloc((size_t)(N + 1) * 4));
+    P.agg = (float*)(ws + alloc((size_t)N * 32 * 4));
+    P.y1b = (unsigned short*)(ws + alloc((size_t)N * 16 * 2));
+    P.hb = (unsigned short*)(ws + alloc((size_t)N * 64 * 2));
+    P.bufA = (float*)(ws + alloc((size_t)N * 64 * 4));
+    P.gs = (float*)(ws + alloc(512 * 4));
+    P.pooled = (float*)(ws + alloc((size_t)(NGRAPHS * 64 + NGRAPHS) * 4));
+    P.cntg = P.pooled + NGRAPHS * 64;
+    P.out = (float*)d_out;
+
+    static int s_grid = -2;
+    if (s_grid == -2) {
+        int dev = 0; hipGetDevice(&dev);
+        int coop = 0; hipDeviceGetAttribute(&coop, hipDeviceAttributeCooperativeLaunch, dev);
+        int cus = 0; hipDeviceGetAttribute(&cus, hipDeviceAttributeMultiprocessorCount, dev);
+        int nb = 0;
+        hipOccupancyMaxActiveBlocksPerMultiprocessor(&nb, (const void*)k_mega, 256, 0);
+        s_grid = (coop && nb > 0 && cus > 0) ? nb * cus : 0;
+        if (s_grid > 2048) s_grid = 2048;
+        if (s_grid < 512) s_grid = 0;
+    }
+
+    if (s_grid > 0) {
+        void* args[] = {(void*)&P};
+        hipError_t e = hipLaunchCooperativeKernel((void*)k_mega, dim3(s_grid), dim3(256), args, 0, stream);
+        if (e == hipSuccess) return;
+        s_grid = 0;
+    }
+
+    w_A<<<1024, 256, 0, stream>>>(P);
+    w_B<<<1, 256, 0, stream>>>(P);
+    w_C<<<NSORT, 256, 0, stream>>>(P);
+    w_D<<<NBUCK, 256, 0, stream>>>(P);
+    w_G16a<<<2048, 256, 0, stream>>>(P);
+    w_L1<<<512, 256, 0, stream>>>(P);
+    w_B1<<<512, 256, 0, stream>>>(P);
+    w_G16b<<<2048, 256, 0, stream>>>(P);
+    w_L2<<<512, 256, 0, stream>>>(P);
+    w_B2<<<512, 256, 0, stream>>>(P);
+    w_G32<<<2048, 256, 0, stream>>>(P);
+    w_L3<<<512, 256, 0, stream>>>(P);
+    w_B3<<<512, 256, 0, stream>>>(P);
+    w_G32<<<2048, 256, 0, stream>>>(P);
+    w_L4<<<512, 256, 0, stream>>>(P);
+    w_P<<<1024, 256, 0, stream>>>(P);
+    w_H<<<1, 256, 0, stream>>>(P);
+}
```

New measurement: 1.778 ms. +178.2%, slower.
